# Kernel tuning notes

Measured on AMD Instinct MI355X. Metric: run time of the kernel, lower is better.

Reference implementation:

```python
import jax, jax.numpy as jnp
import numpy as np

B, LQ, D_MODEL, H, L_CACHE, WINDOW = 4, 512, 2048, 16, 4096, 4096
D_HEAD = D_MODEL // H
EPS = 1e-8


def setup_inputs() -> dict:
    key = jax.random.key(0)
    ks = jax.random.split(key, 9)
    x_chunk = jax.random.normal(ks[0], (B, LQ, D_MODEL), dtype=jnp.float32)
    # int8-range cache values stored as int32 in [-127, 128)
    k_q = jax.random.randint(ks[1], (B, H, L_CACHE, D_HEAD), 0, 255, dtype=jnp.int32) - 127
    v_q = jax.random.randint(ks[2], (B, H, L_CACHE, D_HEAD), 0, 255, dtype=jnp.int32) - 127
    # per-position scales, typical magnitude amax/127
    k_s = jax.random.uniform(ks[3], (B, H, L_CACHE, 1), dtype=jnp.float32, minval=0.005, maxval=0.03)
    v_s = jax.random.uniform(ks[4], (B, H, L_CACHE, 1), dtype=jnp.float32, minval=0.005, maxval=0.03)
    s = 1.0 / np.sqrt(D_MODEL)
    W_q = jax.random.normal(ks[5], (D_MODEL, D_MODEL), dtype=jnp.float32) * s
    W_k = jax.random.normal(ks[6], (D_MODEL, D_MODEL), dtype=jnp.float32) * s
    W_v = jax.random.normal(ks[7], (D_MODEL, D_MODEL), dtype=jnp.float32) * s
    W_o = jax.random.normal(ks[8], (D_MODEL, D_MODEL), dtype=jnp.float32) * s
    return {"x_chunk": x_chunk, "k_q": k_q, "v_q": v_q, "k_s": k_s, "v_s": v_s,
            "W_q": W_q, "W_k": W_k, "W_v": W_v, "W_o": W_o, "window_size": WINDOW}


def _split_heads(x):  # (B, L, d_model) -> (B, H, L, d_head)
    Bb, L, _ = x.shape
    return x.reshape(Bb, L, H, D_HEAD).transpose(0, 2, 1, 3)


def _merge_heads(x):  # (B, H, L, d_head) -> (B, L, d_model)
    Bb, Hh, L, dh = x.shape
    return x.transpose(0, 2, 1, 3).reshape(Bb, L, Hh * dh)


def quantize_int8_lastdim(x):
    amax = jnp.max(jnp.abs(x), axis=-1, keepdims=True)
    scale = jnp.maximum(amax / 127.0, EPS)
    q = jnp.clip(jnp.round(x / scale), -127, 127).astype(jnp.int8)
    return q, scale.astype(jnp.float16)


def reference(x_chunk, k_q, v_q, k_s, v_s, W_q, W_k, W_v, W_o, window_size):
    Lq = x_chunk.shape[1]
    scale = 1.0 / np.sqrt(D_HEAD)
    q = _split_heads(x_chunk @ W_q.T)
    k_new = _split_heads(x_chunk @ W_k.T)
    v_new = _split_heads(x_chunk @ W_v.T)
    # dequantize int8 KV cache: q * scale (per position)
    k_cache = k_q.astype(jnp.float32) * k_s.astype(jnp.float32)
    v_cache = v_q.astype(jnp.float32) * v_s.astype(jnp.float32)
    k_total = jnp.concatenate([k_cache, k_new], axis=2)  # (B,H,Lk,dh)
    v_total = jnp.concatenate([v_cache, v_new], axis=2)
    Lk_total = k_total.shape[2]
    L_cache = k_cache.shape[2]
    # chunked causal mask with cache offset: key j visible to query i iff j <= L_cache + i
    i = jnp.arange(Lq)[:, None]
    j = jnp.arange(Lk_total)[None, :]
    mask = j > (L_cache + i)  # (Lq, Lk)
    attn = jnp.einsum('bhqd,bhkd->bhqk', q, k_total) * scale
    attn = jnp.where(mask[None, None], jnp.finfo(attn.dtype).min, attn)
    attn = jax.nn.softmax(attn, axis=-1)
    y = jnp.einsum('bhqk,bhkd->bhqd', attn, v_total)
    y = _merge_heads(y) @ W_o.T  # (B, Lq, d_model)
    # sliding-window truncation of cache, then re-quantize
    if Lk_total > window_size:
        k_total = k_total[:, :, -window_size:, :]
        v_total = v_total[:, :, -window_size:, :]
    k_tq, k_scale = quantize_int8_lastdim(k_total)
    v_tq, v_scale = quantize_int8_lastdim(v_total)
    return y, k_tq, v_tq, k_scale, v_scale
```

## Files before the change

kernel.cpp:

```cpp
#include <hip/hip_runtime.h>
#include <hip/hip_fp16.h>

typedef float   f32x4   __attribute__((ext_vector_type(4)));
typedef float   f32x2   __attribute__((ext_vector_type(2)));
typedef float   f32x16  __attribute__((ext_vector_type(16)));
typedef short   short8v __attribute__((ext_vector_type(8)));
typedef unsigned short ushort8v __attribute__((ext_vector_type(8)));
typedef unsigned int   u32x4v __attribute__((ext_vector_type(4)));
typedef unsigned int   u32x2v __attribute__((ext_vector_type(2)));
typedef int     int2v   __attribute__((ext_vector_type(2)));
typedef int     int4v   __attribute__((ext_vector_type(4)));
typedef unsigned int   u32;
typedef unsigned short u16;

#define DEVI static __device__ __forceinline__

DEVI u16 f2bf(float f) {
    u32 u = __builtin_bit_cast(u32, f);
    u += 0x7FFFu + ((u >> 16) & 1u);
    return (u16)(u >> 16);
}
DEVI float bf2f(u16 h) { return __builtin_bit_cast(float, (u32)h << 16); }

DEVI void gl_lds16(const u16* g, u16* l) {
    __builtin_amdgcn_global_load_lds(
        (const __attribute__((address_space(1))) u32*)(const void*)g,
        (__attribute__((address_space(3))) u32*)(void*)l, 16, 0, 0);
}

__global__ __launch_bounds__(256) void convert_kernel(
    const float* __restrict__ src, u16* __restrict__ dst, float scale, int n8) {
    int idx = blockIdx.x * 256 + threadIdx.x;
    if (idx >= n8) return;
    const float* p = src + (size_t)idx * 8;
    f32x4 a = *(const f32x4*)p, b = *(const f32x4*)(p + 4);
    ushort8v o;
    o[0]=f2bf(a[0]*scale); o[1]=f2bf(a[1]*scale); o[2]=f2bf(a[2]*scale); o[3]=f2bf(a[3]*scale);
    o[4]=f2bf(b[0]*scale); o[5]=f2bf(b[1]*scale); o[6]=f2bf(b[2]*scale); o[7]=f2bf(b[3]*scale);
    *(ushort8v*)(dst + (size_t)idx * 8) = o;
}

__global__ __launch_bounds__(256) void convert4_kernel(
    const float* __restrict__ x, const float* __restrict__ Wq,
    const float* __restrict__ Wk, const float* __restrict__ Wv,
    u16* __restrict__ xb, u16* __restrict__ wb3, float rscale) {
    const int seg = blockIdx.x >> 11;
    const int idx = (blockIdx.x & 2047) * 256 + threadIdx.x;
    const float* src; u16* dst; float scale = 1.0f;
    if (seg == 0)      { src = x;  dst = xb; }
    else if (seg == 1) { src = Wq; dst = wb3; scale = rscale; }
    else if (seg == 2) { src = Wk; dst = wb3 + 4194304; }
    else               { src = Wv; dst = wb3 + 8388608; }
    const float* p = src + (size_t)idx * 8;
    f32x4 a = *(const f32x4*)p, b = *(const f32x4*)(p + 4);
    ushort8v o;
    o[0]=f2bf(a[0]*scale); o[1]=f2bf(a[1]*scale); o[2]=f2bf(a[2]*scale); o[3]=f2bf(a[3]*scale);
    o[4]=f2bf(b[0]*scale); o[5]=f2bf(b[1]*scale); o[6]=f2bf(b[2]*scale); o[7]=f2bf(b[3]*scale);
    *(ushort8v*)(dst + (size_t)idx * 8) = o;
}

DEVI void prep_body(int pid, char* LB,
    const int* __restrict__ kq, const int* __restrict__ vq,
    const float* __restrict__ ks, const float* __restrict__ vs,
    u16* __restrict__ kcb, u16* __restrict__ vt,
    float* __restrict__ oktq, float* __restrict__ ovtq,
    float* __restrict__ oksc, float* __restrict__ ovsc) {
    u16 (*Vs)[132] = (u16(*)[132])LB;
    float* skL = (float*)(LB + 16896);
    float* svL = (float*)(LB + 17152);
    const int tid = threadIdx.x;
    const int bh = pid >> 6, kt = pid & 63;
    const int key0 = kt << 6;
    const size_t rowbase = (size_t)bh * 4096 + key0;
    if (tid < 64) { skL[tid] = ks[rowbase + tid]; svL[tid] = vs[rowbase + tid]; }
    __syncthreads();
    const int lane = tid & 63, w = tid >> 6;
    const int q31 = lane & 31, rh = lane >> 5;
    u32x2v* kcw = (u32x2v*)kcb;

    int4v kvr[8], vvr[8];
    #pragma unroll
    for (int s = 0; s < 8; ++s) {
        const int key = s * 8 + w * 2 + rh;
        const size_t row = rowbase + key;
        kvr[s] = *(const int4v*)(kq + row * 128 + q31 * 4);
        vvr[s] = *(const int4v*)(vq + row * 128 + q31 * 4);
    }
    #pragma unroll
    for (int s = 0; s < 8; ++s) {
        const int key = s * 8 + w * 2 + rh;
        const float sk = skL[key], sv = svL[key];
        f32x4 kx, vx;
        #pragma unroll
        for (int e = 0; e < 4; ++e) { kx[e] = (float)kvr[s][e] * sk; vx[e] = (float)vvr[s][e] * sv; }
        u32x2v kp, vp;
        kp[0] = (u32)f2bf(kx[0]) | ((u32)f2bf(kx[1]) << 16);
        kp[1] = (u32)f2bf(kx[2]) | ((u32)f2bf(kx[3]) << 16);
        vp[0] = (u32)f2bf(vx[0]) | ((u32)f2bf(vx[1]) << 16);
        vp[1] = (u32)f2bf(vx[2]) | ((u32)f2bf(vx[3]) << 16);
        kcw[(size_t)(bh * 4608 + key0 + key) * 32 + q31] = kp;
        *(u32x2v*)&Vs[key][q31 * 4] = vp;
        float kam = fmaxf(fmaxf(fabsf(kx[0]), fabsf(kx[1])), fmaxf(fabsf(kx[2]), fabsf(kx[3])));
        float vam = fmaxf(fmaxf(fabsf(vx[0]), fabsf(vx[1])), fmaxf(fabsf(vx[2]), fabsf(vx[3])));
        #pragma unroll
        for (int off = 1; off < 32; off <<= 1) {
            kam = fmaxf(kam, __shfl_xor(kam, off, 64));
            vam = fmaxf(vam, __shfl_xor(vam, off, 64));
        }
        const int r = key0 + key;
        if (r >= 512) {
            const size_t orow = (size_t)bh * 4096 + (size_t)(r - 512);
            float kscale = fmaxf(kam / 127.0f, 1e-8f);
            float vscale = fmaxf(vam / 127.0f, 1e-8f);
            float kinv = 1.0f / kscale, vinv = 1.0f / vscale;
            f32x4 ko, vo;
            #pragma unroll
            for (int e = 0; e < 4; ++e) {
                ko[e] = fminf(fmaxf(rintf(kx[e] * kinv), -127.f), 127.f);
                vo[e] = fminf(fmaxf(rintf(vx[e] * vinv), -127.f), 127.f);
            }
            *(f32x4*)(oktq + orow * 128 + q31 * 4) = ko;
            *(f32x4*)(ovtq + orow * 128 + q31 * 4) = vo;
            if (q31 == 0) {
                oksc[orow] = __half2float(__float2half(kscale));
                ovsc[orow] = __half2float(__float2half(vscale));
            }
        }
    }
    __syncthreads();
    const int d = tid >> 1, half = tid & 1;
    u16* obase = vt + ((size_t)bh * 128 + d) * 4608 + key0 + half * 32;
    #pragma unroll
    for (int c = 0; c < 4; ++c) {
        ushort8v tv;
        #pragma unroll
        for (int e = 0; e < 8; ++e) tv[e] = Vs[half * 32 + c * 8 + e][d];
        *(ushort8v*)(obase + c * 8) = tv;
    }
}

DEVI void qkv_body(int qid, char* LB,
    const u16* __restrict__ A, const u16* __restrict__ Bw,
    u16* __restrict__ qbf, u16* __restrict__ kcb, u16* __restrict__ vnb) {
    u16* As = (u16*)LB;
    u16* Bs = (u16*)(LB + 32768);
    const int tid = threadIdx.x, lane = tid & 63, w = tid >> 6;
    const int sid = (qid & 7) * 192 + (qid >> 3);
    const int bm = sid & 15, bn = sid >> 4;
    const int m0 = bm * 128, n0 = bn * 64;
    const int wm = (w >> 1) * 64, wn = (w & 1) * 32;
    const int r16 = lane & 15, kb = lane >> 4;

    f32x4 acc[4][2] = {};

    auto stage = [&](int bi, int k0) {
        #pragma unroll
        for (int i = 0; i < 4; ++i) {
            int s = i * 256 + tid;
            int row = s >> 3, l = (s & 7) ^ (row & 7);
            gl_lds16(A + (size_t)(m0 + row) * 2048 + k0 + l * 8,
                     &As[bi * 8192 + (i * 256 + (tid & ~63)) * 8]);
        }
        #pragma unroll
        for (int i = 0; i < 2; ++i) {
            int s = i * 256 + tid;
            int row = s >> 3, l = (s & 7) ^ (row & 7);
            gl_lds16(Bw + (size_t)(n0 + row) * 2048 + k0 + l * 8,
                     &Bs[bi * 4096 + (i * 256 + (tid & ~63)) * 8]);
        }
    };

    stage(0, 0);
    __syncthreads();
    int cur = 0;
    for (int t = 0; t < 32; ++t) {
        if (t < 31) stage(cur ^ 1, (t + 1) * 64);
        short8v af[4][2], bf[2][2];
        #pragma unroll
        for (int mf = 0; mf < 4; ++mf) {
            int row = wm + mf * 16 + r16;
            #pragma unroll
            for (int ksv = 0; ksv < 2; ++ksv) {
                int blk = (ksv * 4 + kb) ^ (row & 7);
                af[mf][ksv] = __builtin_bit_cast(short8v,
                    *(const ushort8v*)&As[cur * 8192 + row * 64 + blk * 8]);
            }
        }
        #pragma unroll
        for (int nf = 0; nf < 2; ++nf) {
            int row = wn + nf * 16 + r16;
            #pragma unroll
            for (int ksv = 0; ksv < 2; ++ksv) {
                int blk = (ksv * 4 + kb) ^ (row & 7);
                bf[nf][ksv] = __builtin_bit_cast(short8v,
                    *(const ushort8v*)&Bs[cur * 4096 + row * 64 + blk * 8]);
            }
        }
        #pragma unroll
        for (int mf = 0; mf < 4; ++mf)
            #pragma unroll
            for (int nf = 0; nf < 2; ++nf)
                #pragma unroll
                for (int ksv = 0; ksv < 2; ++ksv)
                    acc[mf][nf] = __builtin_amdgcn_mfma_f32_16x16x32_bf16(
                        af[mf][ksv], bf[nf][ksv], acc[mf][nf], 0, 0, 0);
        __syncthreads();
        cur ^= 1;
    }

    #pragma unroll
    for (int mf = 0; mf < 4; ++mf)
        #pragma unroll
        for (int nf = 0; nf < 2; ++nf)
            #pragma unroll
            for (int v = 0; v < 4; ++v) {
                int mg = m0 + wm + mf * 16 + kb * 4 + v;
                int ng = n0 + wn + nf * 16 + r16;
                int nb = ng >> 11, ngl = ng & 2047;
                u16 val = f2bf(acc[mf][nf][v]);
                if (nb == 1) {
                    size_t bh = (size_t)(mg >> 9) * 16 + (ngl >> 7);
                    kcb[(bh * 4608 + 4096 + (mg & 511)) * 128 + (ngl & 127)] = val;
                } else {
                    u16* dst = (nb == 0) ? qbf : vnb;
                    dst[(((size_t)(mg >> 9) * 16 + (ngl >> 7)) * 512 +
                         (mg & 511)) * 128 + (ngl & 127)] = val;
                }
            }
}

__global__ __launch_bounds__(256, 3) void fused_prep_qkv_kernel(
    const int* __restrict__ kq, const int* __restrict__ vq,
    const float* __restrict__ ks, const float* __restrict__ vs,
    u16* __restrict__ kcb, u16* __restrict__ vt,
    float* __restrict__ oktq, float* __restrict__ ovtq,
    float* __restrict__ oksc, float* __restrict__ ovsc,
    const u16* __restrict__ xb, const u16* __restrict__ wb3,
    u16* __restrict__ qbf, u16* __restrict__ vnb) {
    __shared__ __align__(16) char LB[49152];
    const int grp = blockIdx.x / 11, rem = blockIdx.x % 11;
    if (rem < 8) {
        prep_body(grp * 8 + rem, LB, kq, vq, ks, vs, kcb, vt,
                  oktq, ovtq, oksc, ovsc);
    } else {
        qkv_body(grp * 3 + (rem - 8), LB, xb, wb3, qbf, kcb, vnb);
    }
}

__global__ __launch_bounds__(256) void gemm_wo_kernel(
    const u16* __restrict__ A, const u16* __restrict__ Bw,
    float* __restrict__ Cout) {
    __shared__ u16 As[2][128 * 64];
    __shared__ u16 Bs[2][64 * 64];
    const int tid = threadIdx.x, lane = tid & 63, w = tid >> 6;
    const int sid = (blockIdx.x & 7) * 64 + (blockIdx.x >> 3);
    const int bm = sid & 15, bn = sid >> 4;
    const int m0 = bm * 128, n0 = bn * 64;
    const int wm = (w >> 1) * 64, wn = (w & 1) * 32;
    const int r16 = lane & 15, kb = lane >> 4;

    f32x4 acc[4][2] = {};

    auto stage = [&](int bi, int k0) {
        #pragma unroll
        for (int i = 0; i < 4; ++i) {
            int s = i * 256 + tid;
            int row = s >> 3, l = (s & 7) ^ (row & 7);
            gl_lds16(A + (size_t)(m0 + row) * 2048 + k0 + l * 8,
                     &As[bi][(i * 256 + (tid & ~63)) * 8]);
        }
        #pragma unroll
        for (int i = 0; i < 2; ++i) {
            int s = i * 256 + tid;
            int row = s >> 3, l = (s & 7) ^ (row & 7);
            gl_lds16(Bw + (size_t)(n0 + row) * 2048 + k0 + l * 8,
                     &Bs[bi][(i * 256 + (tid & ~63)) * 8]);
        }
    };

    stage(0, 0);
    __syncthreads();
    int cur = 0;
    for (int t = 0; t < 32; ++t) {
        if (t < 31) stage(cur ^ 1, (t + 1) * 64);
        short8v af[4][2], bf[2][2];
        #pragma unroll
        for (int mf = 0; mf < 4; ++mf) {
            int row = wm + mf * 16 + r16;
            #pragma unroll
            for (int ksv = 0; ksv < 2; ++ksv) {
                int blk = (ksv * 4 + kb) ^ (row & 7);
                af[mf][ksv] = __builtin_bit_cast(short8v,
                    *(const ushort8v*)&As[cur][row * 64 + blk * 8]);
            }
        }
        #pragma unroll
        for (int nf = 0; nf < 2; ++nf) {
            int row = wn + nf * 16 + r16;
            #pragma unroll
            for (int ksv = 0; ksv < 2; ++ksv) {
                int blk = (ksv * 4 + kb) ^ (row & 7);
                bf[nf][ksv] = __builtin_bit_cast(short8v,
                    *(const ushort8v*)&Bs[cur][row * 64 + blk * 8]);
            }
        }
        #pragma unroll
        for (int mf = 0; mf < 4; ++mf)
            #pragma unroll
            for (int nf = 0; nf < 2; ++nf)
                #pragma unroll
                for (int ksv = 0; ksv < 2; ++ksv)
                    acc[mf][nf] = __builtin_amdgcn_mfma_f32_16x16x32_bf16(
                        af[mf][ksv], bf[nf][ksv], acc[mf][nf], 0, 0, 0);
        __syncthreads();
        cur ^= 1;
    }

    #pragma unroll
    for (int mf = 0; mf < 4; ++mf)
        #pragma unroll
        for (int nf = 0; nf < 2; ++nf)
            #pragma unroll
            for (int v = 0; v < 4; ++v) {
                int mg = m0 + wm + mf * 16 + kb * 4 + v;
                int ng = n0 + wn + nf * 16 + r16;
                Cout[(size_t)mg * 2048 + ng] = acc[mf][nf][v];
            }
}

__global__ __launch_bounds__(256) void quant_new_kernel(
    const u16* __restrict__ kcb, const u16* __restrict__ vnb,
    u16* __restrict__ vt,
    float* __restrict__ oktq, float* __restrict__ ovtq,
    float* __restrict__ oksc, float* __restrict__ ovsc) {
    __shared__ u16 Vs[64][132];
    const int tid = threadIdx.x;
    const int bh = blockIdx.x >> 3, kt = blockIdx.x & 7;
    const int i0 = kt << 6;
    const int lane = tid & 63, w = tid >> 6;
    const int q31 = lane & 31, rh = lane >> 5;

    u32x2v kur[8], vur[8];
    #pragma unroll
    for (int s = 0; s < 8; ++s) {
        const int key = s * 8 + w * 2 + rh;
        const int i = i0 + key;
        kur[s] = *(const u32x2v*)(kcb + ((size_t)bh * 4608 + 4096 + i) * 128 + q31 * 4);
        vur[s] = *(const u32x2v*)(vnb + ((size_t)bh * 512 + i) * 128 + q31 * 4);
    }
    #pragma unroll
    for (int s = 0; s < 8; ++s) {
        const int key = s * 8 + w * 2 + rh;
        const int i = i0 + key;
        f32x4 kx, vx;
        kx[0] = bf2f((u16)kur[s][0]); kx[1] = bf2f((u16)(kur[s][0] >> 16));
        kx[2] = bf2f((u16)kur[s][1]); kx[3] = bf2f((u16)(kur[s][1] >> 16));
        vx[0] = bf2f((u16)vur[s][0]); vx[1] = bf2f((u16)(vur[s][0] >> 16));
        vx[2] = bf2f((u16)vur[s][1]); vx[3] = bf2f((u16)(vur[s][1] >> 16));
        *(u32x2v*)&Vs[key][q31 * 4] = vur[s];
        float kam = fmaxf(fmaxf(fabsf(kx[0]), fabsf(kx[1])), fmaxf(fabsf(kx[2]), fabsf(kx[3])));
        float vam = fmaxf(fmaxf(fabsf(vx[0]), fabsf(vx[1])), fmaxf(fabsf(vx[2]), fabsf(vx[3])));
        #pragma unroll
        for (int off = 1; off < 32; off <<= 1) {
            kam = fmaxf(kam, __shfl_xor(kam, off, 64));
            vam = fmaxf(vam, __shfl_xor(vam, off, 64));
        }
        float kscale = fmaxf(kam / 127.0f, 1e-8f);
        float vscale = fmaxf(vam / 127.0f, 1e-8f);
        float kinv = 1.0f / kscale, vinv = 1.0f / vscale;
        const size_t orow = (size_t)bh * 4096 + 3584 + i;
        f32x4 ko, vo;
        #pragma unroll
        for (int e = 0; e < 4; ++e) {
            ko[e] = fminf(fmaxf(rintf(kx[e] * kinv), -127.f), 127.f);
            vo[e] = fminf(fmaxf(rintf(vx[e] * vinv), -127.f), 127.f);
        }
        *(f32x4*)(oktq + orow * 128 + q31 * 4) = ko;
        *(f32x4*)(ovtq + orow * 128 + q31 * 4) = vo;
        if (q31 == 0) {
            oksc[orow] = __half2float(__float2half(kscale));
            ovsc[orow] = __half2float(__float2half(vscale));
        }
    }
    __syncthreads();
    const int d = tid >> 1, half = tid & 1;
    u16* obase = vt + ((size_t)bh * 128 + d) * 4608 + 4096 + i0 + half * 32;
    #pragma unroll
    for (int c = 0; c < 4; ++c) {
        ushort8v tv;
        #pragma unroll
        for (int e = 0; e < 8; ++e) tv[e] = Vs[half * 32 + c * 8 + e][d];
        *(ushort8v*)(obase + c * 8) = tv;
    }
}

__global__ __launch_bounds__(256, 3) void attn_kernel(
    const u16* __restrict__ qb, const u16* __restrict__ kcb,
    const u16* __restrict__ vt,
    u16* __restrict__ Op0, u16* __restrict__ Op1, u16* __restrict__ Op2,
    float* __restrict__ mlp) {
    __shared__ u16 Ks[2][32 * 128];
    __shared__ u16 Vl[2][128 * 32];

    const int tid = threadIdx.x, lane = tid & 63, w = tid >> 6;
    const int p = blockIdx.x;
    const int xcd = p & 7, i = p >> 3;
    const int qt2 = i & 3, spw = (i >> 2) % 3;
    const int bh = ((i / 12) << 3) | xcd;
    const int q31 = lane & 31, hi = lane >> 5;
    const int qrow = qt2 * 128 + w * 32 + q31;

    const u16* qp = qb + ((size_t)bh * 512 + qrow) * 128 + hi * 8;
    short8v qf[8];
    #pragma unroll
    for (int s = 0; s < 8; ++s)
        qf[s] = __builtin_bit_cast(short8v, *(const ushort8v*)(qp + s * 16));

    f32x16 O[4] = {};
    float m_i = -3.0e38f, l_i = 0.f;

    const size_t kbase = (size_t)bh * 4608 * 128;
    const size_t vbase = (size_t)bh * 128 * 4608;
    const int e = 132 + 4 * qt2;
    const int ktA = (e * spw) / 3;
    const int ktB = (e * (spw + 1)) / 3;

    auto STAGE = [&](int bi, int kt) {
        #pragma unroll
        for (int ii = 0; ii < 2; ++ii) {
            int s = ii * 256 + tid;
            int row = s >> 4, l = (s & 15) ^ (row & 7);
            gl_lds16(kcb + kbase + (size_t)(kt * 32 + row) * 128 + l * 8,
                     &Ks[bi][(ii * 256 + (tid & ~63)) * 8]);
        }
        #pragma unroll
        for (int ii = 0; ii < 2; ++ii) {
            int s = ii * 256 + tid;
            int row = s >> 2, l = (s & 3) ^ (row & 3);
            gl_lds16(vt + vbase + (size_t)row * 4608 + kt * 32 + l * 8,
                     &Vl[bi][(ii * 256 + (tid & ~63)) * 8]);
        }
    };

    STAGE(0, ktA);
    __syncthreads();
    int cur = 0;
    for (int kt = ktA; kt < ktB; ++kt) {
        if (kt + 1 < ktB) STAGE(cur ^ 1, kt + 1);

        f32x16 S = {};
        __builtin_amdgcn_s_setprio(1);
        #pragma unroll
        for (int s = 0; s < 8; ++s) {
            int blk = (2 * s + hi) ^ (q31 & 7);
            short8v kf = __builtin_bit_cast(short8v,
                *(const ushort8v*)&Ks[cur][q31 * 128 + blk * 8]);
            S = __builtin_amdgcn_mfma_f32_32x32x16_bf16(kf, qf[s], S, 0, 0, 0);
        }
        __builtin_amdgcn_s_setprio(0);

        if (kt >= 128) {
            const int kb0 = (kt - 128) * 32 + 4 * hi;
            #pragma unroll
            for (int r = 0; r < 16; ++r) {
                int koff = kb0 + (r & 3) + 8 * (r >> 2);
                if (koff > qrow) S[r] = -3.0e38f;
            }
        }

        float mx = S[0];
        #pragma unroll
        for (int r = 1; r < 16; ++r) mx = fmaxf(mx, S[r]);
        mx = fmaxf(mx, __shfl_xor(mx, 32, 64));

        if (__ballot(mx > m_i + 8.f)) {
            float mnew = fmaxf(m_i, mx);
            float alpha = __expf(m_i - mnew);
            m_i = mnew;
            l_i *= alpha;
            #pragma unroll
            for (int r = 0; r < 16; ++r) {
                float ar = __shfl(alpha, (r & 3) + 8 * (r >> 2) + 4 * hi, 64);
                O[0][r] *= ar; O[1][r] *= ar; O[2][r] *= ar; O[3][r] *= ar;
            }
        }
        #pragma unroll
        for (int r = 0; r < 16; ++r) {
            S[r] = __expf(S[r] - m_i); l_i += S[r];
        }

        __builtin_amdgcn_s_setprio(1);
        #pragma unroll
        for (int j = 0; j < 2; ++j) {
            const int r0 = 8 * j;
            u32 a0, a1, b0, b1;
            asm("v_cvt_pk_bf16_f32 %0, %1, %2" : "=v"(a0) : "v"(S[r0+0]), "v"(S[r0+1]));
            asm("v_cvt_pk_bf16_f32 %0, %1, %2" : "=v"(a1) : "v"(S[r0+2]), "v"(S[r0+3]));
            asm("v_cvt_pk_bf16_f32 %0, %1, %2" : "=v"(b0) : "v"(S[r0+4]), "v"(S[r0+5]));
            asm("v_cvt_pk_bf16_f32 %0, %1, %2" : "=v"(b1) : "v"(S[r0+6]), "v"(S[r0+7]));
            asm("v_permlane32_swap_b32 %0, %1" : "+v"(a0), "+v"(b0));
            asm("v_permlane32_swap_b32 %0, %1" : "+v"(a1), "+v"(b1));
            u32x4v pw = {a0, a1, b0, b1};
            short8v pf = __builtin_bit_cast(short8v, pw);
            #pragma unroll
            for (int od = 0; od < 4; ++od) {
                int vrow = od * 32 + q31;
                int blk = (2 * j + hi) ^ (vrow & 3);
                short8v vf = __builtin_bit_cast(short8v,
                    *(const ushort8v*)&Vl[cur][vrow * 32 + blk * 8]);
                O[od] = __builtin_amdgcn_mfma_f32_32x32x16_bf16(pf, vf, O[od], 0, 0, 0);
            }
        }
        __builtin_amdgcn_s_setprio(0);

        __syncthreads();
        cur ^= 1;
    }

    float lt = l_i + __shfl_xor(l_i, 32, 64);
    u16* Op = (spw == 0) ? Op0 : ((spw == 1) ? Op1 : Op2);
    const size_t pbase = ((size_t)bh * 4 + qt2) * 16384;
    #pragma unroll
    for (int r = 0; r < 16; ++r) {
        int qoff = (r & 3) + 8 * (r >> 2) + 4 * hi;
        size_t rowb = pbase + (size_t)(w * 32 + qoff) * 128 + q31;
        Op[rowb +  0] = f2bf(O[0][r]);
        Op[rowb + 32] = f2bf(O[1][r]);
        Op[rowb + 64] = f2bf(O[2][r]);
        Op[rowb + 96] = f2bf(O[3][r]);
    }
    if (hi == 0) {
        int qg = ((spw * 256 + bh * 4 + qt2) * 128 + w * 32 + q31);
        mlp[qg * 2 + 0] = m_i;
        mlp[qg * 2 + 1] = lt;
    }
}

__global__ __launch_bounds__(256) void combine_kernel(
    const u16* __restrict__ Op0, const u16* __restrict__ Op1,
    const u16* __restrict__ Op2,
    const float* __restrict__ mlp, u16* __restrict__ yb) {
    const int p = blockIdx.x;
    const int bh = p >> 2, qt2 = p & 3;
    const int b = bh >> 4, h = bh & 15;
    const int q = threadIdx.x >> 1, dh = threadIdx.x & 1;
    const int base = (bh * 4 + qt2) * 128 + q;
    float m0 = mlp[base * 2],               l0 = mlp[base * 2 + 1];
    float m1 = mlp[(32768 + base) * 2],     l1 = mlp[(32768 + base) * 2 + 1];
    float m2 = mlp[(65536 + base) * 2],     l2 = mlp[(65536 + base) * 2 + 1];
    float M = fmaxf(fmaxf(m0, m1), m2);
    float a0 = __expf(m0 - M), a1 = __expf(m1 - M), a2 = __expf(m2 - M);
    float invL = 1.0f / (l0 * a0 + l1 * a1 + l2 * a2);
    a0 *= invL; a1 *= invL; a2 *= invL;
    const size_t pb = ((size_t)bh * 4 + qt2) * 16384 + (size_t)q * 128 + dh * 64;
    u16* dst = yb + ((size_t)(b * 512 + qt2 * 128 + q)) * 2048 + h * 128 + dh * 64;
    #pragma unroll
    for (int j = 0; j < 8; ++j) {
        ushort8v o0 = *(const ushort8v*)(Op0 + pb + j * 8);
        ushort8v o1 = *(const ushort8v*)(Op1 + pb + j * 8);
        ushort8v o2 = *(const ushort8v*)(Op2 + pb + j * 8);
        ushort8v o;
        #pragma unroll
        for (int e = 0; e < 8; ++e)
            o[e] = f2bf(bf2f(o0[e]) * a0 + bf2f(o1[e]) * a1 + bf2f(o2[e]) * a2);
        *(ushort8v*)(dst + j * 8) = o;
    }
}

extern "C" void kernel_launch(void* const* d_in, const int* in_sizes, int n_in,
                              void* d_out, int out_size, void* d_ws, size_t ws_size,
                              hipStream_t stream) {
    (void)in_sizes; (void)n_in; (void)out_size; (void)ws_size;
    const float* x   = (const float*)d_in[0];
    const int*   kq  = (const int*)d_in[1];
    const int*   vq  = (const int*)d_in[2];
    const float* ks  = (const float*)d_in[3];
    const float* vs  = (const float*)d_in[4];
    const float* Wq  = (const float*)d_in[5];
    const float* Wk  = (const float*)d_in[6];
    const float* Wv  = (const float*)d_in[7];
    const float* Wo  = (const float*)d_in[8];

    float* out  = (float*)d_out;
    float* y_o  = out;
    float* oktq = out + 4194304;
    float* ovtq = out + 37748736;
    float* oksc = out + 71303168;
    float* ovsc = out + 71565312;
    float* mlp  = out;

    char* wsb = (char*)d_ws;
    u16* kcb = (u16*)(wsb);
    u16* vtb = (u16*)(wsb + 75497472);
    u16* xb  = (u16*)(wsb + 150994944);
    u16* qbf = (u16*)(wsb + 159383552);
    u16* vnb = (u16*)(wsb + 167772160);
    u16* ybf = (u16*)(wsb + 176160768);
    u16* wb3 = (u16*)(wsb + 184549376);

    const float rscale = 0.08838834764831845f;
    const int n8 = 2048 * 2048 / 8;

    convert4_kernel<<<8192, 256, 0, stream>>>(x, Wq, Wk, Wv, xb, wb3, rscale);
    fused_prep_qkv_kernel<<<5632, 256, 0, stream>>>(
        kq, vq, ks, vs, kcb, vtb, oktq, ovtq, oksc, ovsc,
        xb, wb3, qbf, vnb);
    quant_new_kernel<<<512, 256, 0, stream>>>(kcb, vnb, vtb,
                                              oktq, ovtq, oksc, ovsc);
    attn_kernel<<<768, 256, 0, stream>>>(qbf, kcb, vtb, xb, vnb, ybf, mlp);
    combine_kernel<<<256, 256, 0, stream>>>(xb, vnb, ybf, mlp, qbf);
    convert_kernel<<<2048, 256, 0, stream>>>(Wo, wb3, 1.0f, n8);
    gemm_wo_kernel<<<512, 256, 0, stream>>>(qbf, wb3, y_o);
}
```

Measured before the change: 411.4 us.

## Raise fused prep/QKV occupancy, single-buffer QKV GEMM LDS, fuse Wo convert into combine

```diff
diff --git a/kernel.cpp b/kernel.cpp
--- a/kernel.cpp
+++ b/kernel.cpp
@@ -26,18 +26,6 @@
     __builtin_amdgcn_global_load_lds(
         (const __attribute__((address_space(1))) u32*)(const void*)g,
         (__attribute__((address_space(3))) u32*)(void*)l, 16, 0, 0);
-}
-
-__global__ __launch_bounds__(256) void convert_kernel(
-    const float* __restrict__ src, u16* __restrict__ dst, float scale, int n8) {
-    int idx = blockIdx.x * 256 + threadIdx.x;
-    if (idx >= n8) return;
-    const float* p = src + (size_t)idx * 8;
-    f32x4 a = *(const f32x4*)p, b = *(const f32x4*)(p + 4);
-    ushort8v o;
-    o[0]=f2bf(a[0]*scale); o[1]=f2bf(a[1]*scale); o[2]=f2bf(a[2]*scale); o[3]=f2bf(a[3]*scale);
-    o[4]=f2bf(b[0]*scale); o[5]=f2bf(b[1]*scale); o[6]=f2bf(b[2]*scale); o[7]=f2bf(b[3]*scale);
-    *(ushort8v*)(dst + (size_t)idx * 8) = o;
 }
 
 __global__ __launch_bounds__(256) void convert4_kernel(
@@ -77,22 +65,16 @@
     const int lane = tid & 63, w = tid >> 6;
     const int q31 = lane & 31, rh = lane >> 5;
     u32x2v* kcw = (u32x2v*)kcb;
-
-    int4v kvr[8], vvr[8];
-    #pragma unroll
+    #pragma unroll 4
     for (int s = 0; s < 8; ++s) {
         const int key = s * 8 + w * 2 + rh;
         const size_t row = rowbase + key;
-        kvr[s] = *(const int4v*)(kq + row * 128 + q31 * 4);
-        vvr[s] = *(const int4v*)(vq + row * 128 + q31 * 4);
-    }
-    #pragma unroll
-    for (int s = 0; s < 8; ++s) {
-        const int key = s * 8 + w * 2 + rh;
         const float sk = skL[key], sv = svL[key];
+        int4v kv = *(const int4v*)(kq + row * 128 + q31 * 4);
+        int4v vv = *(const int4v*)(vq + row * 128 + q31 * 4);
         f32x4 kx, vx;
         #pragma unroll
-        for (int e = 0; e < 4; ++e) { kx[e] = (float)kvr[s][e] * sk; vx[e] = (float)vvr[s][e] * sv; }
+        for (int e = 0; e < 4; ++e) { kx[e] = (float)kv[e] * sk; vx[e] = (float)vv[e] * sv; }
         u32x2v kp, vp;
         kp[0] = (u32)f2bf(kx[0]) | ((u32)f2bf(kx[1]) << 16);
         kp[1] = (u32)f2bf(kx[2]) | ((u32)f2bf(kx[3]) << 16);
@@ -143,7 +125,7 @@
     const u16* __restrict__ A, const u16* __restrict__ Bw,
     u16* __restrict__ qbf, u16* __restrict__ kcb, u16* __restrict__ vnb) {
     u16* As = (u16*)LB;
-    u16* Bs = (u16*)(LB + 32768);
+    u16* Bs = (u16*)(LB + 16384);
     const int tid = threadIdx.x, lane = tid & 63, w = tid >> 6;
     const int sid = (qid & 7) * 192 + (qid >> 3);
     const int bm = sid & 15, bn = sid >> 4;
@@ -153,28 +135,23 @@
 
     f32x4 acc[4][2] = {};
 
-    auto stage = [&](int bi, int k0) {
+    for (int t = 0; t < 32; ++t) {
+        const int k0 = t * 64;
         #pragma unroll
         for (int i = 0; i < 4; ++i) {
             int s = i * 256 + tid;
             int row = s >> 3, l = (s & 7) ^ (row & 7);
             gl_lds16(A + (size_t)(m0 + row) * 2048 + k0 + l * 8,
-                     &As[bi * 8192 + (i * 256 + (tid & ~63)) * 8]);
+                     &As[(i * 256 + (tid & ~63)) * 8]);
         }
         #pragma unroll
         for (int i = 0; i < 2; ++i) {
             int s = i * 256 + tid;
             int row = s >> 3, l = (s & 7) ^ (row & 7);
             gl_lds16(Bw + (size_t)(n0 + row) * 2048 + k0 + l * 8,
-                     &Bs[bi * 4096 + (i * 256 + (tid & ~63)) * 8]);
-        }
-    };
-
-    stage(0, 0);
-    __syncthreads();
-    int cur = 0;
-    for (int t = 0; t < 32; ++t) {
-        if (t < 31) stage(cur ^ 1, (t + 1) * 64);
+                     &Bs[(i * 256 + (tid & ~63)) * 8]);
+        }
+        __syncthreads();
         short8v af[4][2], bf[2][2];
         #pragma unroll
         for (int mf = 0; mf < 4; ++mf) {
@@ -183,7 +160,7 @@
             for (int ksv = 0; ksv < 2; ++ksv) {
                 int blk = (ksv * 4 + kb) ^ (row & 7);
                 af[mf][ksv] = __builtin_bit_cast(short8v,
-                    *(const ushort8v*)&As[cur * 8192 + row * 64 + blk * 8]);
+                    *(const ushort8v*)&As[row * 64 + blk * 8]);
             }
         }
         #pragma unroll
@@ -193,7 +170,7 @@
             for (int ksv = 0; ksv < 2; ++ksv) {
                 int blk = (ksv * 4 + kb) ^ (row & 7);
                 bf[nf][ksv] = __builtin_bit_cast(short8v,
-                    *(const ushort8v*)&Bs[cur * 4096 + row * 64 + blk * 8]);
+                    *(const ushort8v*)&Bs[row * 64 + blk * 8]);
             }
         }
         #pragma unroll
@@ -205,7 +182,6 @@
                     acc[mf][nf] = __builtin_amdgcn_mfma_f32_16x16x32_bf16(
                         af[mf][ksv], bf[nf][ksv], acc[mf][nf], 0, 0, 0);
         __syncthreads();
-        cur ^= 1;
     }
 
     #pragma unroll
@@ -229,7 +205,7 @@
             }
 }
 
-__global__ __launch_bounds__(256, 3) void fused_prep_qkv_kernel(
+__global__ __launch_bounds__(256, 6) void fused_prep_qkv_kernel(
     const int* __restrict__ kq, const int* __restrict__ vq,
     const float* __restrict__ ks, const float* __restrict__ vs,
     u16* __restrict__ kcb, u16* __restrict__ vt,
@@ -237,7 +213,7 @@
     float* __restrict__ oksc, float* __restrict__ ovsc,
     const u16* __restrict__ xb, const u16* __restrict__ wb3,
     u16* __restrict__ qbf, u16* __restrict__ vnb) {
-    __shared__ __align__(16) char LB[49152];
+    __shared__ __align__(16) char LB[24576];
     const int grp = blockIdx.x / 11, rem = blockIdx.x % 11;
     if (rem < 8) {
         prep_body(grp * 8 + rem, LB, kq, vq, ks, vs, kcb, vt,
@@ -339,25 +315,18 @@
     const int i0 = kt << 6;
     const int lane = tid & 63, w = tid >> 6;
     const int q31 = lane & 31, rh = lane >> 5;
-
-    u32x2v kur[8], vur[8];
-    #pragma unroll
+    #pragma unroll 4
     for (int s = 0; s < 8; ++s) {
         const int key = s * 8 + w * 2 + rh;
         const int i = i0 + key;
-        kur[s] = *(const u32x2v*)(kcb + ((size_t)bh * 4608 + 4096 + i) * 128 + q31 * 4);
-        vur[s] = *(const u32x2v*)(vnb + ((size_t)bh * 512 + i) * 128 + q31 * 4);
-    }
-    #pragma unroll
-    for (int s = 0; s < 8; ++s) {
-        const int key = s * 8 + w * 2 + rh;
-        const int i = i0 + key;
+        u32x2v ku = *(const u32x2v*)(kcb + ((size_t)bh * 4608 + 4096 + i) * 128 + q31 * 4);
+        u32x2v vu = *(const u32x2v*)(vnb + ((size_t)bh * 512 + i) * 128 + q31 * 4);
         f32x4 kx, vx;
-        kx[0] = bf2f((u16)kur[s][0]); kx[1] = bf2f((u16)(kur[s][0] >> 16));
-        kx[2] = bf2f((u16)kur[s][1]); kx[3] = bf2f((u16)(kur[s][1] >> 16));
-        vx[0] = bf2f((u16)vur[s][0]); vx[1] = bf2f((u16)(vur[s][0] >> 16));
-        vx[2] = bf2f((u16)vur[s][1]); vx[3] = bf2f((u16)(vur[s][1] >> 16));
-        *(u32x2v*)&Vs[key][q31 * 4] = vur[s];
+        kx[0] = bf2f((u16)ku[0]); kx[1] = bf2f((u16)(ku[0] >> 16));
+        kx[2] = bf2f((u16)ku[1]); kx[3] = bf2f((u16)(ku[1] >> 16));
+        vx[0] = bf2f((u16)vu[0]); vx[1] = bf2f((u16)(vu[0] >> 16));
+        vx[2] = bf2f((u16)vu[1]); vx[3] = bf2f((u16)(vu[1] >> 16));
+        *(u32x2v*)&Vs[key][q31 * 4] = vu;
         float kam = fmaxf(fmaxf(fabsf(kx[0]), fabsf(kx[1])), fmaxf(fabsf(kx[2]), fabsf(kx[3])));
         float vam = fmaxf(fmaxf(fabsf(vx[0]), fabsf(vx[1])), fmaxf(fabsf(vx[2]), fabsf(vx[3])));
         #pragma unroll
@@ -536,10 +505,21 @@
     }
 }
 
-__global__ __launch_bounds__(256) void combine_kernel(
+__global__ __launch_bounds__(256) void combine_conv_kernel(
     const u16* __restrict__ Op0, const u16* __restrict__ Op1,
     const u16* __restrict__ Op2,
-    const float* __restrict__ mlp, u16* __restrict__ yb) {
+    const float* __restrict__ mlp, u16* __restrict__ yb,
+    const float* __restrict__ Wo, u16* __restrict__ wb3) {
+    if (blockIdx.x >= 256) {
+        const int idx = (blockIdx.x - 256) * 256 + threadIdx.x;
+        const float* p = Wo + (size_t)idx * 8;
+        f32x4 a = *(const f32x4*)p, b = *(const f32x4*)(p + 4);
+        ushort8v o;
+        o[0]=f2bf(a[0]); o[1]=f2bf(a[1]); o[2]=f2bf(a[2]); o[3]=f2bf(a[3]);
+        o[4]=f2bf(b[0]); o[5]=f2bf(b[1]); o[6]=f2bf(b[2]); o[7]=f2bf(b[3]);
+        *(ushort8v*)(wb3 + (size_t)idx * 8) = o;
+        return;
+    }
     const int p = blockIdx.x;
     const int bh = p >> 2, qt2 = p & 3;
     const int b = bh >> 4, h = bh & 15;
@@ -599,7 +579,6 @@
     u16* wb3 = (u16*)(wsb + 184549376);
 
     const float rscale = 0.08838834764831845f;
-    const int n8 = 2048 * 2048 / 8;
 
     convert4_kernel<<<8192, 256, 0, stream>>>(x, Wq, Wk, Wv, xb, wb3, rscale);
     fused_prep_qkv_kernel<<<5632, 256, 0, stream>>>(
@@ -608,7 +587,7 @@
     quant_new_kernel<<<512, 256, 0, stream>>>(kcb, vnb, vtb,
                                               oktq, ovtq, oksc, ovsc);
     attn_kernel<<<768, 256, 0, stream>>>(qbf, kcb, vtb, xb, vnb, ybf, mlp);
-    combine_kernel<<<256, 256, 0, stream>>>(xb, vnb, ybf, mlp, qbf);
-    convert_kernel<<<2048, 256, 0, stream>>>(Wo, wb3, 1.0f, n8);
+    combine_conv_kernel<<<2304, 256, 0, stream>>>(xb, vnb, ybf, mlp, qbf,
+                                                  Wo, wb3);
     gemm_wo_kernel<<<512, 256, 0, stream>>>(qbf, wb3, y_o);
 }
```

Result: slower. 455.7 us (+10.8%).
